# Optimization experiments

Measured on AMD Instinct MI355X. Metric: run time of the kernel, lower is better.

Reference implementation:

```python
import jax, jax.numpy as jnp
import numpy as np

CLAMP = 2.0
# FrEIA AllInOneBlock global affine init for SOFTPLUS type with global_affine_init=1.0:
# raw param = 2*log(exp(0.5*10*1.0)-1); activation = 0.1 * softplus(beta=0.5)(a) = 0.2*log(1+exp(0.5*a))
GS_INIT = 2.0 * float(np.log(np.exp(5.0) - 1.0))

N = 1_000_000
D = 4          # dQ_feat
DC = 2         # dCond
HID = 64       # hidden_dim
NB = 8         # num_blocks
D1, D2 = D - D // 2, D // 2  # FrEIA split: [2, 2]


def setup_inputs() -> dict:
    key = jax.random.key(0)
    ks = jax.random.split(key, 10)
    q_feat = jax.random.normal(ks[0], (N, D), jnp.float32)
    H = jax.random.normal(ks[1], (N, DC), jnp.float32)
    fin1 = D1 + DC
    W1 = jax.random.normal(ks[2], (NB, HID, fin1), jnp.float32) / jnp.sqrt(fin1)
    b1 = jnp.zeros((NB, HID), jnp.float32)
    W2 = jax.random.normal(ks[3], (NB, HID, HID), jnp.float32) / jnp.sqrt(HID)
    b2 = jnp.zeros((NB, HID), jnp.float32)
    W3 = jax.random.normal(ks[4], (NB, 2 * D2, HID), jnp.float32) / jnp.sqrt(HID)
    b3 = jnp.zeros((NB, 2 * D2), jnp.float32)
    # soft permutation: random orthogonal matrix per block (fixed, like special_ortho_group)
    w_perm = jax.vmap(lambda k: jnp.linalg.qr(jax.random.normal(k, (D, D), jnp.float32))[0])(
        jax.random.split(ks[5], NB))
    g_scale = jnp.full((NB, D), GS_INIT, jnp.float32)
    g_offset = jnp.zeros((NB, D), jnp.float32)
    return {"q_feat": q_feat, "H": H, "W1": W1, "b1": b1, "W2": W2, "b2": b2,
            "W3": W3, "b3": b3, "w_perm": w_perm, "g_scale": g_scale, "g_offset": g_offset}


def reference(q_feat, H, W1, b1, W2, b2, W3, b3, w_perm, g_scale, g_offset):
    x = q_feat
    logdet = jnp.zeros(x.shape[0], x.dtype)
    n_blocks = W1.shape[0]
    for i in range(n_blocks):
        x1, x2 = x[:, :D1], x[:, D1:]
        x1c = jnp.concatenate([x1, H], axis=1)                     # [N, D1+DC]
        h = jax.nn.relu(x1c @ W1[i].T + b1[i])                     # [N, HID]
        h = jax.nn.relu(h @ W2[i].T + b2[i])
        a = (h @ W3[i].T + b3[i]) * 0.1                            # [N, 2*D2]
        s = CLAMP * jnp.tanh(a[:, :D2])                            # clamped log-scale
        t = a[:, D2:]
        x2 = x2 * jnp.exp(s) + t
        j = jnp.sum(s, axis=1)
        x = jnp.concatenate([x1, x2], axis=1)
        # global affine + soft permutation (F.linear(x, w_perm) == x @ w_perm.T)
        scale = 0.2 * jnp.log1p(jnp.exp(0.5 * g_scale[i]))         # 0.1 * softplus(beta=0.5)
        x = (x * scale + g_offset[i]) @ w_perm[i].T
        logdet = logdet + j + jnp.sum(jnp.log(scale))
    return x, logdet
```

## Files before the change

### kernel.cpp

```cpp
#include <hip/hip_runtime.h>

typedef _Float16 f16;
typedef _Float16 f16x8 __attribute__((ext_vector_type(8)));
typedef float f32x4 __attribute__((ext_vector_type(4)));
typedef uint32_t u32x4 __attribute__((ext_vector_type(4)));

#define NBLK 8
#define NS 3
#define NIMG 14
#define MFMA(a, b, c) __builtin_amdgcn_mfma_f32_16x16x32_f16(a, b, c, 0, 0, 0)
#define LOG2E 1.4426950408889634f

__device__ __forceinline__ int pinv(int k) {
  return 16 * (2 * (k >> 5) + ((k >> 2) & 1)) + 4 * ((k >> 3) & 3) + (k & 3);
}
__device__ __forceinline__ float hi_part(float v) { return (float)(f16)v; }
__device__ __forceinline__ float lo_part(float v) { f16 h = (f16)v; return v - (float)h; }

__device__ __forceinline__ float fast_exp2(float x) {
  float r; asm("v_exp_f32 %0, %1" : "=v"(r) : "v"(x)); return r;
}
__device__ __forceinline__ float fast_rcp(float x) {
  float r; asm("v_rcp_f32 %0, %1" : "=v"(r) : "v"(x)); return r;
}
__device__ __forceinline__ uint32_t pkrtz_u(float a, float b) {
  auto p = __builtin_amdgcn_cvt_pkrtz(a, b);
  return __builtin_bit_cast(uint32_t, p);
}
__device__ __forceinline__ uint32_t mix_lo_pk(uint32_t hi_pk, float neg1,
                                              float r0, float r1) {
  uint32_t d;
  asm("v_fma_mixlo_f16 %0, %1, %2, %3 op_sel:[0,0,0] op_sel_hi:[1,0,0]\n\t"
      "v_fma_mixhi_f16 %0, %1, %2, %4 op_sel:[1,0,0] op_sel_hi:[1,0,0]"
      : "=&v"(d)
      : "v"(hi_pk), "v"(neg1), "v"(r0), "v"(r1));
  return d;
}

__global__ void prep_weights(const float* __restrict__ W1, const float* __restrict__ b1,
                             const float* __restrict__ W2, const float* __restrict__ W3,
                             const float* __restrict__ b3, const float* __restrict__ w_perm,
                             const float* __restrict__ g_scale, const float* __restrict__ g_offset,
                             f16* __restrict__ wsp, float* __restrict__ cwp) {
  int i = blockIdx.x / (NIMG + 1);
  int img = blockIdx.x % (NIMG + 1);
  if (img == NIMG) {
    int tid = threadIdx.x;
    if (tid < 16) {
      int cc = tid & 3;
      float gs = g_scale[i * 4 + cc];
      float sc = 0.2f * log1pf(expf(0.5f * gs));
      cwp[i * 24 + tid] = w_perm[i * 16 + tid] * sc;
    } else if (tid < 20) {
      int r = tid - 16;
      float acc = 0.f;
      for (int cc = 0; cc < 4; ++cc)
        acc += w_perm[i * 16 + r * 4 + cc] * g_offset[i * 4 + cc];
      cwp[i * 24 + 16 + r] = acc;
    } else if (tid < 24) {
      int j = tid - 20;
      float scale = (j < 2) ? (0.2f * LOG2E) : 0.1f;
      cwp[i * 24 + 20 + j] = b3[i * 4 + j] * scale;
    } else if (tid == 24 && i == 0) {
      float acc = 0.f;
      for (int k = 0; k < 32; ++k)
        acc += logf(0.2f * log1pf(expf(0.5f * g_scale[k])));
      cwp[192] = acc;
    }
    return;
  }
  int lane = threadIdx.x;
  int c = lane & 15, g = lane >> 4;
  f16 vals[8];
#pragma unroll
  for (int e = 0; e < 8; ++e) {
    float out = 0.f;
    if (img < 4) {
      int t = img, m = 16 * t + c, k = 8 * g + e;
      if (k < 4)        out = hi_part(W1[i * 256 + m * 4 + k]);
      else if (k < 8)   out = lo_part(W1[i * 256 + m * 4 + (k - 4)]);
      else if (k < 12)  out = hi_part(W1[i * 256 + m * 4 + (k - 8)]);
      else if (k == 12) out = hi_part(b1[i * 64 + m]);
      else if (k == 13) out = lo_part(b1[i * 64 + m]);
      else out = 0.f;
    } else if (img < 12) {
      int q = img - 4;
      int t = q >> 1, s = q & 1, m = 16 * t + c;
      int k = 32 * s + 8 * g + e;
      out = hi_part(W2[i * 4096 + m * 64 + pinv(k)]);
    } else {
      int s = img - 12;
      int k = 32 * s + 8 * g + e;
      int rr = c & 3;
      float rs = (rr < 2) ? (0.2f * LOG2E) : 0.1f;
      out = hi_part(W3[i * 256 + rr * 64 + pinv(k)] * rs);
    }
    vals[e] = (f16)out;
  }
  f16x8 vv = {vals[0], vals[1], vals[2], vals[3], vals[4], vals[5], vals[6], vals[7]};
  *(f16x8*)(wsp + ((size_t)i * NIMG + img) * 512 + (size_t)lane * 8) = vv;
}

__device__ __forceinline__ f16x8 make_bh(const f32x4 d0, const f32x4 d1,
                                         uint32_t zero_u) {
  u32x4 u;
  u[0] = pkrtz_u(d0[0], d0[1]);
  u[1] = pkrtz_u(d0[2], d0[3]);
  u[2] = pkrtz_u(d1[0], d1[1]);
  u[3] = pkrtz_u(d1[2], d1[3]);
#pragma unroll
  for (int p = 0; p < 4; ++p) {
    uint32_t r;
    asm("v_pk_max_f16 %0, %1, %2" : "=v"(r) : "v"(u[p]), "v"(zero_u));
    u[p] = r;
  }
  return __builtin_bit_cast(f16x8, u);
}

struct Pt {
  float x0, x1, x2, x3, ld;
  uint32_t ch_pk, cl_pk;
};

__device__ __forceinline__ f16x8 build_B1(const Pt& s, bool g0, bool g1, float neg1) {
  const uint32_t ones_pk = 0x3C003C00u;
  uint32_t xh_pk = pkrtz_u(s.x0, s.x1);
  uint32_t xl_pk = mix_lo_pk(xh_pk, neg1, s.x0, s.x1);
  u32x4 B1u = {g0 ? xh_pk : (g1 ? xl_pk : 0u),
               g0 ? s.ch_pk : (g1 ? s.cl_pk : 0u),
               g0 ? xh_pk : (g1 ? ones_pk : 0u),
               g0 ? s.ch_pk : 0u};
  return __builtin_bit_cast(f16x8, B1u);
}

__device__ __forceinline__ void couple(Pt& st, const f32x4 d3,
                                       const float* __restrict__ cw) {
  float a0 = d3[0] + cw[20];
  float a1 = d3[1] + cw[21];
  float t2 = d3[2] + cw[22];
  float t3 = d3[3] + cw[23];
  float u0 = fast_exp2(a0), u1 = fast_exp2(a1);
  float s0 = fmaf(-4.f, fast_rcp(u0 + 1.f), 2.f);
  float s1 = fmaf(-4.f, fast_rcp(u1 + 1.f), 2.f);
  float e0 = fast_exp2(s0 * LOG2E), e1 = fast_exp2(s1 * LOG2E);
  st.x2 = fmaf(st.x2, e0, t2);
  st.x3 = fmaf(st.x3, e1, t3);
  st.ld += s0 + s1;
  float nx0 = fmaf(st.x0, cw[0],  fmaf(st.x1, cw[1],  fmaf(st.x2, cw[2],  fmaf(st.x3, cw[3],  cw[16]))));
  float nx1 = fmaf(st.x0, cw[4],  fmaf(st.x1, cw[5],  fmaf(st.x2, cw[6],  fmaf(st.x3, cw[7],  cw[17]))));
  float nx2 = fmaf(st.x0, cw[8],  fmaf(st.x1, cw[9],  fmaf(st.x2, cw[10], fmaf(st.x3, cw[11], cw[18]))));
  float nx3 = fmaf(st.x0, cw[12], fmaf(st.x1, cw[13], fmaf(st.x2, cw[14], fmaf(st.x3, cw[15], cw[19]))));
  st.x0 = nx0; st.x1 = nx1; st.x2 = nx2; st.x3 = nx3;
}

__global__ __launch_bounds__(256) void cinn_mfma_kernel(
    const float* __restrict__ q_feat, const float* __restrict__ Hc,
    const float* __restrict__ b2, const f16* __restrict__ wf,
    const float* __restrict__ cwp,
    float* __restrict__ out_x, float* __restrict__ out_ld, int n) {
  int lane = threadIdx.x & 63;
  int c = lane & 15, g = lane >> 4;
  bool g0 = (g == 0), g1 = (g == 1);
  int wave = (blockIdx.x * blockDim.x + threadIdx.x) >> 6;
  float neg1 = -1.0f;
  uint32_t zero_u = 0u;

  int pt[NS];
  Pt st[NS];
#pragma unroll
  for (int u = 0; u < NS; ++u) {
    int p = wave * (16 * NS) + u * 16 + c;
    if (p >= n) p = n - 1;
    pt[u] = p;
    float4 xv = *reinterpret_cast<const float4*>(q_feat + (size_t)p * 4);
    st[u].x0 = xv.x; st[u].x1 = xv.y; st[u].x2 = xv.z; st[u].x3 = xv.w;
    st[u].ld = 0.f;
    float2 hv = *reinterpret_cast<const float2*>(Hc + (size_t)p * 2);
    st[u].ch_pk = pkrtz_u(hv.x, hv.y);
    st[u].cl_pk = mix_lo_pk(st[u].ch_pk, neg1, hv.x, hv.y);
  }

  const f32x4 zero4 = {0.f, 0.f, 0.f, 0.f};

#pragma unroll 1
  for (int i = 0; i < NBLK; ++i) {
    const f16* wb = wf + (size_t)i * NIMG * 512 + (size_t)lane * 8;
    const float* cw = cwp + i * 24;

    f16x8 B1[NS];
#pragma unroll
    for (int u = 0; u < NS; ++u) B1[u] = build_B1(st[u], g0, g1, neg1);

    f16x8 b2h[NS][2];
#pragma unroll
    for (int half = 0; half < 2; ++half) {
      f32x4 dp[NS][2];
#pragma unroll
      for (int tt = 0; tt < 2; ++tt) {
        f16x8 a = *(const f16x8*)(wb + (2 * half + tt) * 512);
#pragma unroll
        for (int u = 0; u < NS; ++u) dp[u][tt] = MFMA(a, B1[u], zero4);
      }
#pragma unroll
      for (int u = 0; u < NS; ++u)
        b2h[u][half] = make_bh(dp[u][0], dp[u][1], zero_u);
    }

    f16x8 b3h[NS][2];
#pragma unroll
    for (int half = 0; half < 2; ++half) {
      f32x4 d2[NS][2];
#pragma unroll
      for (int tt = 0; tt < 2; ++tt) {
        int t = 2 * half + tt;
        f16x8 ah0 = *(const f16x8*)(wb + (4 + 2 * t + 0) * 512);
        f16x8 ah1 = *(const f16x8*)(wb + (4 + 2 * t + 1) * 512);
        const float4 bv = *reinterpret_cast<const float4*>(b2 + i * 64 + 16 * t + 4 * g);
        f32x4 cin = {bv.x, bv.y, bv.z, bv.w};
#pragma unroll
        for (int u = 0; u < NS; ++u) {
          f32x4 acc = MFMA(ah0, b2h[u][0], cin);
          acc = MFMA(ah1, b2h[u][1], acc);
          d2[u][tt] = acc;
        }
      }
#pragma unroll
      for (int u = 0; u < NS; ++u)
        b3h[u][half] = make_bh(d2[u][0], d2[u][1], zero_u);
    }

    f32x4 d3[NS];
    {
      f16x8 ah0 = *(const f16x8*)(wb + 12 * 512);
      f16x8 ah1 = *(const f16x8*)(wb + 13 * 512);
#pragma unroll
      for (int u = 0; u < NS; ++u) {
        f32x4 acc = MFMA(ah0, b3h[u][0], zero4);
        acc = MFMA(ah1, b3h[u][1], acc);
        d3[u] = acc;
      }
    }

#pragma unroll
    for (int u = 0; u < NS; ++u) couple(st[u], d3[u], cw);
  }

  if (lane < 16) {
    float lt = cwp[192];
#pragma unroll
    for (int u = 0; u < NS; ++u) {
      *reinterpret_cast<float4*>(out_x + (size_t)pt[u] * 4) =
          make_float4(st[u].x0, st[u].x1, st[u].x2, st[u].x3);
      out_ld[pt[u]] = st[u].ld + lt;
    }
  }
}

extern "C" void kernel_launch(void* const* d_in, const int* in_sizes, int n_in,
                              void* d_out, int out_size, void* d_ws, size_t ws_size,
                              hipStream_t stream) {
  const float* q_feat   = (const float*)d_in[0];
  const float* Hc       = (const float*)d_in[1];
  const float* W1       = (const float*)d_in[2];
  const float* b1       = (const float*)d_in[3];
  const float* W2       = (const float*)d_in[4];
  const float* b2       = (const float*)d_in[5];
  const float* W3       = (const float*)d_in[6];
  const float* b3       = (const float*)d_in[7];
  const float* w_perm   = (const float*)d_in[8];
  const float* g_scale  = (const float*)d_in[9];
  const float* g_offset = (const float*)d_in[10];

  int n = in_sizes[0] / 4;
  float* out_x  = (float*)d_out;
  float* out_ld = out_x + (size_t)n * 4;
  f16* wf = (f16*)d_ws;
  float* cwp = (float*)((char*)d_ws + 114688);

  hipLaunchKernelGGL(prep_weights, dim3(NBLK * (NIMG + 1)), dim3(64), 0, stream,
                     W1, b1, W2, W3, b3, w_perm, g_scale, g_offset, wf, cwp);
  int ppb = 256 / 64 * 16 * NS;
  int blocks = (n + ppb - 1) / ppb;
  hipLaunchKernelGGL(cinn_mfma_kernel, dim3(blocks), dim3(256), 0, stream,
                     q_feat, Hc, b2, wf, cwp, out_x, out_ld, n);
}
```

Baseline: 161.0 us.

## Switch MLP to 32x32x16 MFMA tiles with 32 points per wave

Moves the per-point MLP from 16x16x32 MFMAs over three interleaved 16-point slices to 32x32x16 MFMAs over one 32-point column set per wave. The weight images and the b2 bias are re-laid out in prep to match the 32x32 operand layout. This aims to raise MFMA throughput per instruction and cut weight-fragment loads. In exchange each wave holds fewer independent chains (32 points instead of 48), which lowers ILP for hiding MFMA latency and needs more waves in total.

```diff
diff --git a/kernel.cpp b/kernel.cpp
--- a/kernel.cpp
+++ b/kernel.cpp
@@ -3,16 +3,16 @@
 typedef _Float16 f16;
 typedef _Float16 f16x8 __attribute__((ext_vector_type(8)));
 typedef float f32x4 __attribute__((ext_vector_type(4)));
+typedef float f32x16 __attribute__((ext_vector_type(16)));
 typedef uint32_t u32x4 __attribute__((ext_vector_type(4)));
 
 #define NBLK 8
-#define NS 3
 #define NIMG 14
-#define MFMA(a, b, c) __builtin_amdgcn_mfma_f32_16x16x32_f16(a, b, c, 0, 0, 0)
+#define MFMA32(a, b, c) __builtin_amdgcn_mfma_f32_32x32x16_f16(a, b, c, 0, 0, 0)
 #define LOG2E 1.4426950408889634f
 
-__device__ __forceinline__ int pinv(int k) {
-  return 16 * (2 * (k >> 5) + ((k >> 2) & 1)) + 4 * ((k >> 3) & 3) + (k & 3);
+__device__ __forceinline__ int pinv32(int j, int k) {
+  return 32 * (j >> 1) + (k & 3) + 8 * (2 * (j & 1) + ((k >> 2) & 1)) + 4 * (k >> 3);
 }
 __device__ __forceinline__ float hi_part(float v) { return (float)(f16)v; }
 __device__ __forceinline__ float lo_part(float v) { f16 h = (f16)v; return v - (float)h; }
@@ -39,9 +39,11 @@
 
 __global__ void prep_weights(const float* __restrict__ W1, const float* __restrict__ b1,
                              const float* __restrict__ W2, const float* __restrict__ W3,
-                             const float* __restrict__ b3, const float* __restrict__ w_perm,
+                             const float* __restrict__ b2, const float* __restrict__ b3,
+                             const float* __restrict__ w_perm,
                              const float* __restrict__ g_scale, const float* __restrict__ g_offset,
-                             f16* __restrict__ wsp, float* __restrict__ cwp) {
+                             f16* __restrict__ wsp, float* __restrict__ cwp,
+                             float* __restrict__ cwp2) {
   int i = blockIdx.x / (NIMG + 1);
   int img = blockIdx.x % (NIMG + 1);
   if (img == NIMG) {
@@ -67,33 +69,37 @@
         acc += logf(0.2f * log1pf(expf(0.5f * g_scale[k])));
       cwp[192] = acc;
     }
+    {
+      int T2 = threadIdx.x >> 5, hi = (threadIdx.x >> 4) & 1, r = threadIdx.x & 15;
+      cwp2[i * 64 + threadIdx.x] =
+          b2[i * 64 + 32 * T2 + (r & 3) + 8 * (r >> 2) + 4 * hi];
+    }
     return;
   }
   int lane = threadIdx.x;
-  int c = lane & 15, g = lane >> 4;
+  int row = lane & 31, hi = lane >> 5;
   f16 vals[8];
 #pragma unroll
   for (int e = 0; e < 8; ++e) {
+    int k = 8 * hi + e;
     float out = 0.f;
-    if (img < 4) {
-      int t = img, m = 16 * t + c, k = 8 * g + e;
+    if (img < 2) {
+      int m = 32 * img + row;
       if (k < 4)        out = hi_part(W1[i * 256 + m * 4 + k]);
       else if (k < 8)   out = lo_part(W1[i * 256 + m * 4 + (k - 4)]);
       else if (k < 12)  out = hi_part(W1[i * 256 + m * 4 + (k - 8)]);
       else if (k == 12) out = hi_part(b1[i * 64 + m]);
       else if (k == 13) out = lo_part(b1[i * 64 + m]);
       else out = 0.f;
-    } else if (img < 12) {
-      int q = img - 4;
-      int t = q >> 1, s = q & 1, m = 16 * t + c;
-      int k = 32 * s + 8 * g + e;
-      out = hi_part(W2[i * 4096 + m * 64 + pinv(k)]);
+    } else if (img < 10) {
+      int q = img - 2, T2 = q >> 2, j = q & 3;
+      int m = 32 * T2 + row;
+      out = hi_part(W2[i * 4096 + m * 64 + pinv32(j, k)]);
     } else {
-      int s = img - 12;
-      int k = 32 * s + 8 * g + e;
-      int rr = c & 3;
+      int j = img - 10;
+      int rr = row & 3;
       float rs = (rr < 2) ? (0.2f * LOG2E) : 0.1f;
-      out = hi_part(W3[i * 256 + rr * 64 + pinv(k)] * rs);
+      out = hi_part(W3[i * 256 + rr * 64 + pinv32(j, k)] * rs);
     }
     vals[e] = (f16)out;
   }
@@ -101,13 +107,13 @@
   *(f16x8*)(wsp + ((size_t)i * NIMG + img) * 512 + (size_t)lane * 8) = vv;
 }
 
-__device__ __forceinline__ f16x8 make_bh(const f32x4 d0, const f32x4 d1,
-                                         uint32_t zero_u) {
+template <int OFF>
+__device__ __forceinline__ f16x8 cvt_relu(const f32x16 d, uint32_t zero_u) {
   u32x4 u;
-  u[0] = pkrtz_u(d0[0], d0[1]);
-  u[1] = pkrtz_u(d0[2], d0[3]);
-  u[2] = pkrtz_u(d1[0], d1[1]);
-  u[3] = pkrtz_u(d1[2], d1[3]);
+  u[0] = pkrtz_u(d[OFF + 0], d[OFF + 1]);
+  u[1] = pkrtz_u(d[OFF + 2], d[OFF + 3]);
+  u[2] = pkrtz_u(d[OFF + 4], d[OFF + 5]);
+  u[3] = pkrtz_u(d[OFF + 6], d[OFF + 7]);
 #pragma unroll
   for (int p = 0; p < 4; ++p) {
     uint32_t r;
@@ -117,142 +123,90 @@
   return __builtin_bit_cast(f16x8, u);
 }
 
-struct Pt {
-  float x0, x1, x2, x3, ld;
-  uint32_t ch_pk, cl_pk;
-};
-
-__device__ __forceinline__ f16x8 build_B1(const Pt& s, bool g0, bool g1, float neg1) {
-  const uint32_t ones_pk = 0x3C003C00u;
-  uint32_t xh_pk = pkrtz_u(s.x0, s.x1);
-  uint32_t xl_pk = mix_lo_pk(xh_pk, neg1, s.x0, s.x1);
-  u32x4 B1u = {g0 ? xh_pk : (g1 ? xl_pk : 0u),
-               g0 ? s.ch_pk : (g1 ? s.cl_pk : 0u),
-               g0 ? xh_pk : (g1 ? ones_pk : 0u),
-               g0 ? s.ch_pk : 0u};
-  return __builtin_bit_cast(f16x8, B1u);
-}
-
-__device__ __forceinline__ void couple(Pt& st, const f32x4 d3,
-                                       const float* __restrict__ cw) {
-  float a0 = d3[0] + cw[20];
-  float a1 = d3[1] + cw[21];
-  float t2 = d3[2] + cw[22];
-  float t3 = d3[3] + cw[23];
-  float u0 = fast_exp2(a0), u1 = fast_exp2(a1);
-  float s0 = fmaf(-4.f, fast_rcp(u0 + 1.f), 2.f);
-  float s1 = fmaf(-4.f, fast_rcp(u1 + 1.f), 2.f);
-  float e0 = fast_exp2(s0 * LOG2E), e1 = fast_exp2(s1 * LOG2E);
-  st.x2 = fmaf(st.x2, e0, t2);
-  st.x3 = fmaf(st.x3, e1, t3);
-  st.ld += s0 + s1;
-  float nx0 = fmaf(st.x0, cw[0],  fmaf(st.x1, cw[1],  fmaf(st.x2, cw[2],  fmaf(st.x3, cw[3],  cw[16]))));
-  float nx1 = fmaf(st.x0, cw[4],  fmaf(st.x1, cw[5],  fmaf(st.x2, cw[6],  fmaf(st.x3, cw[7],  cw[17]))));
-  float nx2 = fmaf(st.x0, cw[8],  fmaf(st.x1, cw[9],  fmaf(st.x2, cw[10], fmaf(st.x3, cw[11], cw[18]))));
-  float nx3 = fmaf(st.x0, cw[12], fmaf(st.x1, cw[13], fmaf(st.x2, cw[14], fmaf(st.x3, cw[15], cw[19]))));
-  st.x0 = nx0; st.x1 = nx1; st.x2 = nx2; st.x3 = nx3;
-}
-
 __global__ __launch_bounds__(256) void cinn_mfma_kernel(
     const float* __restrict__ q_feat, const float* __restrict__ Hc,
-    const float* __restrict__ b2, const f16* __restrict__ wf,
-    const float* __restrict__ cwp,
+    const f16* __restrict__ wf, const float* __restrict__ cwp,
+    const float* __restrict__ cwp2,
     float* __restrict__ out_x, float* __restrict__ out_ld, int n) {
   int lane = threadIdx.x & 63;
-  int c = lane & 15, g = lane >> 4;
-  bool g0 = (g == 0), g1 = (g == 1);
+  int col = lane & 31;
+  bool h0 = (lane < 32);
   int wave = (blockIdx.x * blockDim.x + threadIdx.x) >> 6;
   float neg1 = -1.0f;
   uint32_t zero_u = 0u;
-
-  int pt[NS];
-  Pt st[NS];
-#pragma unroll
-  for (int u = 0; u < NS; ++u) {
-    int p = wave * (16 * NS) + u * 16 + c;
-    if (p >= n) p = n - 1;
-    pt[u] = p;
-    float4 xv = *reinterpret_cast<const float4*>(q_feat + (size_t)p * 4);
-    st[u].x0 = xv.x; st[u].x1 = xv.y; st[u].x2 = xv.z; st[u].x3 = xv.w;
-    st[u].ld = 0.f;
-    float2 hv = *reinterpret_cast<const float2*>(Hc + (size_t)p * 2);
-    st[u].ch_pk = pkrtz_u(hv.x, hv.y);
-    st[u].cl_pk = mix_lo_pk(st[u].ch_pk, neg1, hv.x, hv.y);
-  }
-
-  const f32x4 zero4 = {0.f, 0.f, 0.f, 0.f};
+  const uint32_t ones_pk = 0x3C003C00u;
+
+  int p = wave * 32 + col;
+  if (p >= n) p = n - 1;
+  float4 xv = *reinterpret_cast<const float4*>(q_feat + (size_t)p * 4);
+  float x0 = xv.x, x1 = xv.y, x2 = xv.z, x3 = xv.w;
+  float ld = 0.f;
+  float2 hv = *reinterpret_cast<const float2*>(Hc + (size_t)p * 2);
+  uint32_t ch_pk = pkrtz_u(hv.x, hv.y);
+  uint32_t cl_pk = mix_lo_pk(ch_pk, neg1, hv.x, hv.y);
+
+  const f32x16 zero16 = {0.f, 0.f, 0.f, 0.f, 0.f, 0.f, 0.f, 0.f,
+                         0.f, 0.f, 0.f, 0.f, 0.f, 0.f, 0.f, 0.f};
 
 #pragma unroll 1
   for (int i = 0; i < NBLK; ++i) {
     const f16* wb = wf + (size_t)i * NIMG * 512 + (size_t)lane * 8;
     const float* cw = cwp + i * 24;
 
-    f16x8 B1[NS];
+    uint32_t xh_pk = pkrtz_u(x0, x1);
+    uint32_t xl_pk = mix_lo_pk(xh_pk, neg1, x0, x1);
+    u32x4 B1u = {h0 ? xh_pk : xl_pk,
+                 h0 ? ch_pk : cl_pk,
+                 h0 ? xh_pk : ones_pk,
+                 h0 ? ch_pk : 0u};
+    f16x8 B1 = __builtin_bit_cast(f16x8, B1u);
+
+    f32x16 d1a = MFMA32(*(const f16x8*)(wb + 0 * 512), B1, zero16);
+    f32x16 d1b = MFMA32(*(const f16x8*)(wb + 1 * 512), B1, zero16);
+    f16x8 bf[4];
+    bf[0] = cvt_relu<0>(d1a, zero_u);
+    bf[1] = cvt_relu<8>(d1a, zero_u);
+    bf[2] = cvt_relu<0>(d1b, zero_u);
+    bf[3] = cvt_relu<8>(d1b, zero_u);
+
+    f16x8 b3f[4];
 #pragma unroll
-    for (int u = 0; u < NS; ++u) B1[u] = build_B1(st[u], g0, g1, neg1);
-
-    f16x8 b2h[NS][2];
-#pragma unroll
-    for (int half = 0; half < 2; ++half) {
-      f32x4 dp[NS][2];
-#pragma unroll
-      for (int tt = 0; tt < 2; ++tt) {
-        f16x8 a = *(const f16x8*)(wb + (2 * half + tt) * 512);
-#pragma unroll
-        for (int u = 0; u < NS; ++u) dp[u][tt] = MFMA(a, B1[u], zero4);
-      }
-#pragma unroll
-      for (int u = 0; u < NS; ++u)
-        b2h[u][half] = make_bh(dp[u][0], dp[u][1], zero_u);
-    }
-
-    f16x8 b3h[NS][2];
-#pragma unroll
-    for (int half = 0; half < 2; ++half) {
-      f32x4 d2[NS][2];
-#pragma unroll
-      for (int tt = 0; tt < 2; ++tt) {
-        int t = 2 * half + tt;
-        f16x8 ah0 = *(const f16x8*)(wb + (4 + 2 * t + 0) * 512);
-        f16x8 ah1 = *(const f16x8*)(wb + (4 + 2 * t + 1) * 512);
-        const float4 bv = *reinterpret_cast<const float4*>(b2 + i * 64 + 16 * t + 4 * g);
-        f32x4 cin = {bv.x, bv.y, bv.z, bv.w};
-#pragma unroll
-        for (int u = 0; u < NS; ++u) {
-          f32x4 acc = MFMA(ah0, b2h[u][0], cin);
-          acc = MFMA(ah1, b2h[u][1], acc);
-          d2[u][tt] = acc;
-        }
-      }
-#pragma unroll
-      for (int u = 0; u < NS; ++u)
-        b3h[u][half] = make_bh(d2[u][0], d2[u][1], zero_u);
-    }
-
-    f32x4 d3[NS];
-    {
-      f16x8 ah0 = *(const f16x8*)(wb + 12 * 512);
-      f16x8 ah1 = *(const f16x8*)(wb + 13 * 512);
-#pragma unroll
-      for (int u = 0; u < NS; ++u) {
-        f32x4 acc = MFMA(ah0, b3h[u][0], zero4);
-        acc = MFMA(ah1, b3h[u][1], acc);
-        d3[u] = acc;
-      }
-    }
-
-#pragma unroll
-    for (int u = 0; u < NS; ++u) couple(st[u], d3[u], cw);
-  }
-
-  if (lane < 16) {
-    float lt = cwp[192];
-#pragma unroll
-    for (int u = 0; u < NS; ++u) {
-      *reinterpret_cast<float4*>(out_x + (size_t)pt[u] * 4) =
-          make_float4(st[u].x0, st[u].x1, st[u].x2, st[u].x3);
-      out_ld[pt[u]] = st[u].ld + lt;
-    }
+    for (int T2 = 0; T2 < 2; ++T2) {
+      const f32x16 cin = *(const f32x16*)(cwp2 + i * 64 + T2 * 32 + (h0 ? 0 : 16));
+      f32x16 acc = MFMA32(*(const f16x8*)(wb + (2 + T2 * 4 + 0) * 512), bf[0], cin);
+      acc = MFMA32(*(const f16x8*)(wb + (2 + T2 * 4 + 1) * 512), bf[1], acc);
+      acc = MFMA32(*(const f16x8*)(wb + (2 + T2 * 4 + 2) * 512), bf[2], acc);
+      acc = MFMA32(*(const f16x8*)(wb + (2 + T2 * 4 + 3) * 512), bf[3], acc);
+      b3f[2 * T2 + 0] = cvt_relu<0>(acc, zero_u);
+      b3f[2 * T2 + 1] = cvt_relu<8>(acc, zero_u);
+    }
+
+    f32x16 d3 = MFMA32(*(const f16x8*)(wb + 10 * 512), b3f[0], zero16);
+    d3 = MFMA32(*(const f16x8*)(wb + 11 * 512), b3f[1], d3);
+    d3 = MFMA32(*(const f16x8*)(wb + 12 * 512), b3f[2], d3);
+    d3 = MFMA32(*(const f16x8*)(wb + 13 * 512), b3f[3], d3);
+
+    float a0 = d3[0] + cw[20];
+    float a1 = d3[1] + cw[21];
+    float t2 = d3[2] + cw[22];
+    float t3 = d3[3] + cw[23];
+    float u0 = fast_exp2(a0), u1 = fast_exp2(a1);
+    float s0 = fmaf(-4.f, fast_rcp(u0 + 1.f), 2.f);
+    float s1 = fmaf(-4.f, fast_rcp(u1 + 1.f), 2.f);
+    float e0 = fast_exp2(s0 * LOG2E), e1 = fast_exp2(s1 * LOG2E);
+    x2 = fmaf(x2, e0, t2);
+    x3 = fmaf(x3, e1, t3);
+    ld += s0 + s1;
+    float nx0 = fmaf(x0, cw[0],  fmaf(x1, cw[1],  fmaf(x2, cw[2],  fmaf(x3, cw[3],  cw[16]))));
+    float nx1 = fmaf(x0, cw[4],  fmaf(x1, cw[5],  fmaf(x2, cw[6],  fmaf(x3, cw[7],  cw[17]))));
+    float nx2 = fmaf(x0, cw[8],  fmaf(x1, cw[9],  fmaf(x2, cw[10], fmaf(x3, cw[11], cw[18]))));
+    float nx3 = fmaf(x0, cw[12], fmaf(x1, cw[13], fmaf(x2, cw[14], fmaf(x3, cw[15], cw[19]))));
+    x0 = nx0; x1 = nx1; x2 = nx2; x3 = nx3;
+  }
+
+  if (lane < 32) {
+    *reinterpret_cast<float4*>(out_x + (size_t)p * 4) = make_float4(x0, x1, x2, x3);
+    out_ld[p] = ld + cwp[192];
   }
 }
 
@@ -275,12 +229,13 @@
   float* out_x  = (float*)d_out;
   float* out_ld = out_x + (size_t)n * 4;
   f16* wf = (f16*)d_ws;
-  float* cwp = (float*)((char*)d_ws + 114688);
+  float* cwp  = (float*)((char*)d_ws + 114688);
+  float* cwp2 = (float*)((char*)d_ws + 115712);
 
   hipLaunchKernelGGL(prep_weights, dim3(NBLK * (NIMG + 1)), dim3(64), 0, stream,
-                     W1, b1, W2, W3, b3, w_perm, g_scale, g_offset, wf, cwp);
-  int ppb = 256 / 64 * 16 * NS;
-  int blocks = (n + ppb - 1) / ppb;
+                     W1, b1, W2, W3, b2, b3, w_perm, g_scale, g_offset,
+                     wf, cwp, cwp2);
+  int blocks = (n + 127) / 128;
   hipLaunchKernelGGL(cinn_mfma_kernel, dim3(blocks), dim3(256), 0, stream,
-                     q_feat, Hc, b2, wf, cwp, out_x, out_ld, n);
-}
+                     q_feat, Hc, wf, cwp, cwp2, out_x, out_ld, n);
+}
```

Measured after the change: 185.7 us. 1.15x slower.
